# Kernel tuning notes

Measured on AMD Instinct MI355X. Metric: run time of the kernel, lower is better.

Reference implementation:

```python
import jax, jax.numpy as jnp
import numpy as np

THRESHOLD = 0.5
NEG_POS_RATIO = 3
ALPHA = 10.0
N_PRIORS = 8732
N_CLASSES = 21
BATCH = 128
N_OBJ = 32


def cxcy_to_xy(cxcy):
    return jnp.concatenate([cxcy[..., :2] - cxcy[..., 2:] / 2.0,
                            cxcy[..., :2] + cxcy[..., 2:] / 2.0], axis=-1)


def xy_to_cxcy(xy):
    return jnp.concatenate([(xy[..., :2] + xy[..., 2:]) / 2.0,
                            xy[..., 2:] - xy[..., :2]], axis=-1)


def cxcy_to_gcxgcy(cxcy, priors_cxcy):
    return jnp.concatenate([(cxcy[..., :2] - priors_cxcy[..., :2]) / (priors_cxcy[..., 2:] / 10.0),
                            jnp.log(cxcy[..., 2:] / priors_cxcy[..., 2:]) * 5.0], axis=-1)


def find_jaccard_overlap(a, b):
    # a: (M,4) xyxy, b: (P,4) xyxy -> (M,P)
    lt = jnp.maximum(a[:, None, :2], b[None, :, :2])
    rb = jnp.minimum(a[:, None, 2:], b[None, :, 2:])
    wh = jnp.clip(rb - lt, 0.0)
    inter = wh[..., 0] * wh[..., 1]
    area_a = (a[:, 2] - a[:, 0]) * (a[:, 3] - a[:, 1])
    area_b = (b[:, 2] - b[:, 0]) * (b[:, 3] - b[:, 1])
    return inter / (area_a[:, None] + area_b[None, :] - inter)


def _match_one(boxes, labels, priors_xy, priors_cxcy):
    # boxes: (M,4) xyxy, labels: (M,)
    iou = find_jaccard_overlap(boxes, priors_xy)           # (M,P)
    obj_idx = jnp.argmax(iou, axis=1)                      # best prior per object
    iou = iou.at[jnp.arange(boxes.shape[0]), obj_idx].set(1.0)
    positive = (iou >= THRESHOLD).any(axis=0)              # (P,)
    max_prior_idx = jnp.argmax(iou, axis=0)                # best object per prior
    true_cls = labels[max_prior_idx] * positive.astype(labels.dtype)
    matched = boxes[max_prior_idx]                         # (P,4)
    true_locs = cxcy_to_gcxgcy(xy_to_cxcy(matched), priors_cxcy)
    return true_locs, true_cls, positive


def setup_inputs() -> dict:
    key = jax.random.key(0)
    k1, k2, k3, k4, k5, k6 = jax.random.split(key, 6)
    pred_loc = jax.random.normal(k1, (BATCH, N_PRIORS, 4), dtype=jnp.float32)
    pred_cls = jax.random.normal(k2, (BATCH, N_PRIORS, N_CLASSES), dtype=jnp.float32)
    # valid xyxy gt boxes in [0,1]
    p1 = jax.random.uniform(k3, (BATCH, N_OBJ, 2))
    p2 = jax.random.uniform(k4, (BATCH, N_OBJ, 2))
    b_boxes = jnp.concatenate([jnp.minimum(p1, p2), jnp.maximum(p1, p2) + 1e-3], axis=-1)
    b_boxes = jnp.clip(b_boxes, 0.0, 1.0).astype(jnp.float32)
    b_labels = jax.random.randint(k5, (BATCH, N_OBJ), 1, N_CLASSES)
    cxy = jax.random.uniform(k6, (N_PRIORS, 2), minval=0.1, maxval=0.9)
    wh = jax.random.uniform(jax.random.fold_in(k6, 1), (N_PRIORS, 2), minval=0.05, maxval=0.3)
    priors_cxcy = jnp.concatenate([cxy, wh], axis=-1).astype(jnp.float32)
    return {"pred_loc": pred_loc, "pred_cls": pred_cls, "b_boxes": b_boxes,
            "b_labels": b_labels, "priors_cxcy": priors_cxcy}


def reference(pred_loc, pred_cls, b_boxes, b_labels, priors_cxcy):
    batch_size, n_priors, n_classes = pred_cls.shape
    priors_xy = cxcy_to_xy(priors_cxcy)
    true_locs, true_classes, positive = jax.vmap(
        _match_one, in_axes=(0, 0, None, None))(b_boxes, b_labels, priors_xy, priors_cxcy)
    pos_f = positive.astype(pred_loc.dtype)                 # (B,P)
    n_positives = positive.sum(axis=1)                      # (B,)
    n_pos_total = n_positives.sum().astype(pred_loc.dtype)
    # L1 loss (mean over positive box elements)
    loc_loss = (jnp.abs(pred_loc - true_locs) * pos_f[..., None]).sum() / (n_pos_total * 4.0)
    # per-prior cross-entropy
    logp = jax.nn.log_softmax(pred_cls, axis=-1)
    ce = -jnp.take_along_axis(logp, true_classes[..., None], axis=-1)[..., 0]  # (B,P)
    conf_loss_pos = (ce * pos_f).sum()
    # hard negative mining: sort negatives descending per image
    conf_neg = jnp.where(positive, 0.0, ce)
    conf_neg_sorted = -jnp.sort(-conf_neg, axis=1)
    ranks = jnp.arange(n_priors)[None, :]
    hard_mask = ranks < (NEG_POS_RATIO * n_positives)[:, None]
    conf_loss_hard_neg = jnp.where(hard_mask, conf_neg_sorted, 0.0).sum()
    conf_loss = (conf_loss_hard_neg + conf_loss_pos) / n_pos_total
    loc_loss = ALPHA * loc_loss
    total_loss = conf_loss + loc_loss
    return total_loss, loc_loss, conf_loss
```

## Files before the change

### kernel.cpp

```cpp
#include <hip/hip_runtime.h>
#include <math.h>

#define B 128
#define M 32
#define P 8732
#define C 21
#define ALPHA 10.0f
#define NB2 35
#define NSUB 140
#define CH 8
#define CS 1092

typedef float fx4 __attribute__((ext_vector_type(4)));
typedef fx4 fx4u __attribute__((aligned(4)));

#define CE1(val, idx) { float xv_ = (val); se += __expf(xv_); if (cls == (idx)) vc = xv_; }

__global__ __launch_bounds__(256) void k1_partial(
    const float* __restrict__ b_boxes, const float* __restrict__ priors,
    float* __restrict__ pI, float* __restrict__ pU, int* __restrict__ pidx,
    int* __restrict__ done) {
  if (blockIdx.x == 0 && threadIdx.x == 0) *done = 0;
  int b = blockIdx.x >> 3;
  int ch = blockIdx.x & 7;
  int wid = threadIdx.x >> 6;
  int lane = threadIdx.x & 63;
  int obase = wid * 8;

  float ox1[8], oy1[8], ox2[8], oy2[8], oarea[8], bI[8], bU[8];
  int bidx[8];
#pragma unroll
  for (int k = 0; k < 8; k++) {
    float4 bx = ((const float4*)b_boxes)[(size_t)b * M + obase + k];
    ox1[k] = bx.x; oy1[k] = bx.y; ox2[k] = bx.z; oy2[k] = bx.w;
    oarea[k] = (bx.z - bx.x) * (bx.w - bx.y);
    bI[k] = -1.0f; bU[k] = 1.0f; bidx[k] = P;
  }

  int pend = (ch + 1) * CS;
  if (pend > P) pend = P;
#pragma unroll 2
  for (int p = ch * CS + lane; p < pend; p += 64) {
    float4 pr = ((const float4*)priors)[p];
    float pw2 = pr.z * 0.5f, ph2 = pr.w * 0.5f;
    float px1 = pr.x - pw2, py1 = pr.y - ph2;
    float px2 = pr.x + pw2, py2 = pr.y + ph2;
    float areaP = pr.z * pr.w;
#pragma unroll
    for (int k = 0; k < 8; k++) {
      float iw = fminf(ox2[k], px2) - fmaxf(ox1[k], px1);
      float ih = fminf(oy2[k], py2) - fmaxf(oy1[k], py1);
      iw = fmaxf(iw, 0.0f);
      ih = fmaxf(ih, 0.0f);
      float inter = iw * ih;
      float uni = oarea[k] + areaP - inter;
      if (inter * bU[k] > bI[k] * uni) { bI[k] = inter; bU[k] = uni; bidx[k] = p; }
    }
  }
  for (int off = 32; off >= 1; off >>= 1) {
#pragma unroll
    for (int k = 0; k < 8; k++) {
      float oI = __shfl_xor(bI[k], off, 64);
      float oU = __shfl_xor(bU[k], off, 64);
      int oi = __shfl_xor(bidx[k], off, 64);
      float l = oI * bU[k], r = bI[k] * oU;
      if (l > r || (l == r && oi < bidx[k])) { bI[k] = oI; bU[k] = oU; bidx[k] = oi; }
    }
  }
  if (lane == 0) {
#pragma unroll
    for (int k = 0; k < 8; k++) {
      int idx = ((size_t)b * M + obase + k) * CH + ch;
      pI[idx] = bI[k]; pU[idx] = bU[k]; pidx[idx] = bidx[k];
    }
  }
}

template <int KN>
__device__ __forceinline__ void phaseA_group(
    int b, int wid, int lane, int koff, int ntw,
    const float* __restrict__ pred_loc, const float* __restrict__ pred_cls,
    const float* __restrict__ priors,
    const float4* sbox, const int* slab, const int* sobj,
    float* s, float* psl, float* psc, int* psn) {
  float x1[KN], y1[KN], x2[KN], y2[KN], ap[KN];
  float bIr[KN], bUr[KN];
  int bmr[KN], fmr[KN];
#pragma unroll
  for (int j = 0; j < KN; j++) {
    int k = koff + j;
    int p = ((wid + (k << 4)) << 6) + lane;
    x1[j] = 0.0f; y1[j] = 0.0f; x2[j] = 0.0f; y2[j] = 0.0f; ap[j] = 0.0f;
    bIr[j] = -1.0f; bUr[j] = 1.0f; bmr[j] = 0; fmr[j] = 0x7fffffff;
    if (k < ntw && p < P) {
      float4 pr = ((const float4*)priors)[p];
      float pw2 = pr.z * 0.5f, ph2 = pr.w * 0.5f;
      x1[j] = pr.x - pw2; y1[j] = pr.y - ph2;
      x2[j] = pr.x + pw2; y2[j] = pr.y + ph2;
      ap[j] = pr.z * pr.w;
    }
  }
  for (int m = 0; m < M; m++) {
    float4 bx = sbox[m];
    float areaB = (bx.z - bx.x) * (bx.w - bx.y);
    int objm = sobj[m];
#pragma unroll
    for (int j = 0; j < KN; j++) {
      float iw = fminf(bx.z, x2[j]) - fmaxf(bx.x, x1[j]);
      float ih = fminf(bx.w, y2[j]) - fmaxf(bx.y, y1[j]);
      iw = fmaxf(iw, 0.0f);
      ih = fmaxf(ih, 0.0f);
      float inter = iw * ih;
      float uni = areaB + ap[j] - inter;
      if (inter * bUr[j] > bIr[j] * uni) { bIr[j] = inter; bUr[j] = uni; bmr[j] = m; }
      int p = ((wid + ((koff + j) << 4)) << 6) + lane;
      if (fmr[j] == 0x7fffffff && objm == p) fmr[j] = m;
    }
  }
#pragma unroll
  for (int j = 0; j < KN; j++) {
    int k = koff + j;
    if (k < ntw) {
      int t = wid + (k << 4);
      int p = (t << 6) + lane;
      float locpart = 0.0f, cepospart = 0.0f;
      int npos = 0;
      if (p < P) {
        float bIv = bIr[j], bUv = bUr[j];
        int bmv = bmr[j], fmv = fmr[j];
        if (fmv != 0x7fffffff) {
          if (!((bIv == bUv) && (bmv < fmv))) { bIv = 1.0f; bUv = 1.0f; bmv = fmv; }
        }
        bool pos = (2.0f * bIv >= bUv);
        int wAny = __any((int)pos);
        if (wAny) {
          float4 pr = ((const float4*)priors)[p];
          float4 plv = ((const float4*)pred_loc)[(size_t)b * P + p];
          float4 bx = sbox[bmv];
          float cx = (bx.x + bx.z) * 0.5f, cy = (bx.y + bx.w) * 0.5f;
          float w = bx.z - bx.x, h = bx.w - bx.y;
          float rz = __builtin_amdgcn_rcpf(pr.z);
          float rw = __builtin_amdgcn_rcpf(pr.w);
          float g0 = (cx - pr.x) * 10.0f * rz;
          float g1 = (cy - pr.y) * 10.0f * rw;
          float g2 = __logf(w * rz) * 5.0f;
          float g3 = __logf(h * rw) * 5.0f;
          if (pos) {
            locpart = fabsf(plv.x - g0) + fabsf(plv.y - g1) +
                      fabsf(plv.z - g2) + fabsf(plv.w - g3);
            npos = 1;
          }
        }
        int cls = pos ? slab[bmv] : 0;
        const float* uu = pred_cls + ((size_t)b * P + p) * C;
        const fx4u* u4 = (const fx4u*)uu;
        fx4 a0 = u4[0], a1 = u4[1], a2 = u4[2], a3 = u4[3], a4 = u4[4];
        float v20 = uu[20];
        float se = 0.0f, vc = 0.0f;
        CE1(a0.x, 0)  CE1(a0.y, 1)  CE1(a0.z, 2)  CE1(a0.w, 3)
        CE1(a1.x, 4)  CE1(a1.y, 5)  CE1(a1.z, 6)  CE1(a1.w, 7)
        CE1(a2.x, 8)  CE1(a2.y, 9)  CE1(a2.z, 10) CE1(a2.w, 11)
        CE1(a3.x, 12) CE1(a3.y, 13) CE1(a3.z, 14) CE1(a3.w, 15)
        CE1(a4.x, 16) CE1(a4.y, 17) CE1(a4.z, 18) CE1(a4.w, 19)
        CE1(v20, 20)
        float ce = __logf(se) - vc;
        s[p] = pos ? 0.0f : ce;
        cepospart = pos ? ce : 0.0f;
      }
      for (int off = 32; off >= 1; off >>= 1) {
        locpart += __shfl_down(locpart, off, 64);
        cepospart += __shfl_down(cepospart, off, 64);
        npos += __shfl_down(npos, off, 64);
      }
      if (lane == 0) { psl[t] = locpart; psc[t] = cepospart; psn[t] = npos; }
    }
  }
}

__global__ __launch_bounds__(1024) void k23_img(
    const float* __restrict__ pred_loc, const float* __restrict__ pred_cls,
    const float* __restrict__ b_boxes, const int* __restrict__ b_labels,
    const float* __restrict__ priors,
    const float* __restrict__ pI, const float* __restrict__ pU,
    const int* __restrict__ pidx,
    float* __restrict__ imgres, int* __restrict__ done,
    float* __restrict__ out) {
  int b = blockIdx.x;
  int tid = threadIdx.x;
  int wid = tid >> 6;
  int lane = tid & 63;

  __shared__ __align__(16) float s[P];
  __shared__ __align__(16) float4 sbox[M];
  __shared__ int slab[M], sobj[M];
  __shared__ float psl[NSUB], psc[NSUB];
  __shared__ int psn[NSUB];
  __shared__ int histw[16 * 256];
  __shared__ __align__(16) int cnt[256];
  __shared__ int sdig, scum, sK, sLast;
  __shared__ float sLoc, sCe, sNp;
  __shared__ float rsum[16], rl[16], rc[16], rh[16], rn[16];
  __shared__ int rcnt[16];

  if (tid < M) {
    int m = tid;
    float4 bx = ((const float4*)b_boxes)[b * M + m];
    sbox[m] = bx;
    slab[m] = b_labels[b * M + m];
    int o = b * M + m;
    float cI = pI[o * CH], cU = pU[o * CH];
    int ci = pidx[o * CH];
#pragma unroll
    for (int ch = 1; ch < CH; ch++) {
      float nI = pI[o * CH + ch], nU = pU[o * CH + ch];
      int ni = pidx[o * CH + ch];
      if (nI * cU > cI * nU) { cI = nI; cU = nU; ci = ni; }
    }
    sobj[m] = ci;
  }
  __syncthreads();

  int ntw = (wid < 12) ? 9 : 8;
  phaseA_group<5>(b, wid, lane, 0, ntw, pred_loc, pred_cls, priors,
                  sbox, slab, sobj, s, psl, psc, psn);
  phaseA_group<4>(b, wid, lane, 5, ntw, pred_loc, pred_cls, priors,
                  sbox, slab, sobj, s, psl, psc, psn);
  __syncthreads();

  if (wid == 0) {
    float lp = 0.0f, cp = 0.0f;
    int np = 0;
    if (lane < NB2) {
      int t4 = lane * 4;
      lp = ((psl[t4] + psl[t4 + 1]) + psl[t4 + 2]) + psl[t4 + 3];
      cp = ((psc[t4] + psc[t4 + 1]) + psc[t4 + 2]) + psc[t4 + 3];
      np = psn[t4] + psn[t4 + 1] + psn[t4 + 2] + psn[t4 + 3];
    }
    for (int off = 32; off >= 1; off >>= 1) {
      lp += __shfl_down(lp, off, 64);
      cp += __shfl_down(cp, off, 64);
      np += __shfl_down(np, off, 64);
    }
    if (lane == 0) {
      int K = np * 3;
      if (K > P) K = P;
      sK = K; sLoc = lp; sCe = cp; sNp = (float)np;
    }
  }
  __syncthreads();

  int K = sK;
  unsigned pfx = 0;
  int Krem = K;
#pragma unroll
  for (int pass = 3; pass >= 0; --pass) {
    int sh = pass * 8;
    for (int i = tid; i < 16 * 256; i += 1024) histw[i] = 0;
    __syncthreads();
    unsigned himask = (pass == 3) ? 0u : (0xFFFFFFFFu << (sh + 8));
    int* myh = &histw[wid * 256];
    for (int i = tid; i < P; i += 1024) {
      unsigned ub = __float_as_uint(s[i]);
      if ((ub & himask) == pfx) atomicAdd(&myh[(ub >> sh) & 255], 1);
    }
    __syncthreads();
    if (tid < 256) {
      int c = 0;
#pragma unroll
      for (int w = 0; w < 16; w++) c += histw[w * 256 + tid];
      cnt[tid] = c;
    }
    __syncthreads();
    if (wid == 0) {
      int4 c4 = ((const int4*)cnt)[lane];
      int s3 = c4.w;
      int s2 = c4.z + s3;
      int s1 = c4.y + s2;
      int s0 = c4.x + s1;
      int suf = s0;
      for (int off = 1; off < 64; off <<= 1) {
        int t = __shfl_down(suf, off, 64);
        if (lane + off < 64) suf += t;
      }
      int above = suf - s0;
      int S0 = above + s0, S1 = above + s1, S2 = above + s2, S3 = above + s3;
      int S4 = above;
      if (S3 >= Krem && S4 < Krem) { sdig = 4 * lane + 3; scum = S4; }
      else if (S2 >= Krem && S3 < Krem) { sdig = 4 * lane + 2; scum = S3; }
      else if (S1 >= Krem && S2 < Krem) { sdig = 4 * lane + 1; scum = S2; }
      else if (S0 >= Krem && S1 < Krem) { sdig = 4 * lane + 0; scum = S1; }
    }
    __syncthreads();
    pfx |= ((unsigned)sdig) << sh;
    Krem -= scum;
  }
  float tau = __uint_as_float(pfx);

  float sum = 0.0f;
  int cgt = 0;
  for (int i = tid; i < P; i += 1024) {
    float v = s[i];
    if (v > tau) { sum += v; cgt++; }
  }
  for (int off = 32; off >= 1; off >>= 1) {
    sum += __shfl_down(sum, off, 64);
    cgt += __shfl_down(cgt, off, 64);
  }
  if (lane == 0) { rsum[wid] = sum; rcnt[wid] = cgt; }
  __syncthreads();
  if (tid == 0) {
    float stot = 0.0f;
    int ctot = 0;
#pragma unroll
    for (int w = 0; w < 16; w++) { stot += rsum[w]; ctot += rcnt[w]; }
    float hard = stot + (float)(K - ctot) * tau;
    imgres[b * 4 + 0] = sLoc;
    imgres[b * 4 + 1] = sCe;
    imgres[b * 4 + 2] = hard;
    imgres[b * 4 + 3] = sNp;
    __threadfence();
    int prev = atomicAdd(done, 1);
    sLast = (prev == B - 1) ? 1 : 0;
  }
  __syncthreads();
  if (sLast) {
    __threadfence();
    float l = 0.0f, c = 0.0f, h = 0.0f, n = 0.0f;
    if (tid < B) {
      l = atomicAdd(&imgres[tid * 4 + 0], 0.0f);
      c = atomicAdd(&imgres[tid * 4 + 1], 0.0f);
      h = atomicAdd(&imgres[tid * 4 + 2], 0.0f);
      n = atomicAdd(&imgres[tid * 4 + 3], 0.0f);
    }
    for (int off = 32; off >= 1; off >>= 1) {
      l += __shfl_down(l, off, 64);
      c += __shfl_down(c, off, 64);
      h += __shfl_down(h, off, 64);
      n += __shfl_down(n, off, 64);
    }
    if (lane == 0) { rl[wid] = l; rc[wid] = c; rh[wid] = h; rn[wid] = n; }
    __syncthreads();
    if (tid == 0) {
      float L = 0, Cc = 0, H = 0, N = 0;
#pragma unroll
      for (int w = 0; w < 16; w++) { L += rl[w]; Cc += rc[w]; H += rh[w]; N += rn[w]; }
      float loc = ALPHA * L / (N * 4.0f);
      float conf = (H + Cc) / N;
      out[0] = conf + loc;
      out[1] = loc;
      out[2] = conf;
    }
  }
}

extern "C" void kernel_launch(void* const* d_in, const int* in_sizes, int n_in,
                              void* d_out, int out_size, void* d_ws, size_t ws_size,
                              hipStream_t stream) {
  (void)in_sizes; (void)n_in; (void)out_size; (void)ws_size;
  const float* pred_loc = (const float*)d_in[0];
  const float* pred_cls = (const float*)d_in[1];
  const float* b_boxes = (const float*)d_in[2];
  const int* b_labels = (const int*)d_in[3];
  const float* priors = (const float*)d_in[4];
  float* out = (float*)d_out;

  int* done = (int*)d_ws;
  float* imgres = (float*)d_ws + 8;
  float* pI = imgres + B * 4;
  float* pU = pI + B * M * CH;
  int* pidx = (int*)(pU + B * M * CH);

  k1_partial<<<B * CH, 256, 0, stream>>>(b_boxes, priors, pI, pU, pidx, done);
  k23_img<<<B, 1024, 0, stream>>>(pred_loc, pred_cls, b_boxes, b_labels,
                                  priors, pI, pU, pidx, imgres, done, out);
}
```

Baseline: 228.3 us.

## Fuse per-object best-prior search into image kernel and prefetch class logits early

Moves the per-object argmax-over-priors search from a separate 1024-block kernel into the per-image kernel. Partial results now go through shared memory instead of a global workspace, and a tiny init kernel resets the done counter. The pred_cls rows are now loaded up front alongside the priors, before the 32-object IoU loop, so their latency overlaps with compute. Phase A groups are split 3/3/3 to hold the prefetched registers. The risks are higher register pressure and only 128 blocks doing the IoU search, with less parallelism than the old separate kernel.

After: 264.3 us. 15.7% more time.

```diff
diff --git a/kernel.cpp b/kernel.cpp
--- a/kernel.cpp
+++ b/kernel.cpp
@@ -16,64 +16,8 @@
 
 #define CE1(val, idx) { float xv_ = (val); se += __expf(xv_); if (cls == (idx)) vc = xv_; }
 
-__global__ __launch_bounds__(256) void k1_partial(
-    const float* __restrict__ b_boxes, const float* __restrict__ priors,
-    float* __restrict__ pI, float* __restrict__ pU, int* __restrict__ pidx,
-    int* __restrict__ done) {
-  if (blockIdx.x == 0 && threadIdx.x == 0) *done = 0;
-  int b = blockIdx.x >> 3;
-  int ch = blockIdx.x & 7;
-  int wid = threadIdx.x >> 6;
-  int lane = threadIdx.x & 63;
-  int obase = wid * 8;
-
-  float ox1[8], oy1[8], ox2[8], oy2[8], oarea[8], bI[8], bU[8];
-  int bidx[8];
-#pragma unroll
-  for (int k = 0; k < 8; k++) {
-    float4 bx = ((const float4*)b_boxes)[(size_t)b * M + obase + k];
-    ox1[k] = bx.x; oy1[k] = bx.y; ox2[k] = bx.z; oy2[k] = bx.w;
-    oarea[k] = (bx.z - bx.x) * (bx.w - bx.y);
-    bI[k] = -1.0f; bU[k] = 1.0f; bidx[k] = P;
-  }
-
-  int pend = (ch + 1) * CS;
-  if (pend > P) pend = P;
-#pragma unroll 2
-  for (int p = ch * CS + lane; p < pend; p += 64) {
-    float4 pr = ((const float4*)priors)[p];
-    float pw2 = pr.z * 0.5f, ph2 = pr.w * 0.5f;
-    float px1 = pr.x - pw2, py1 = pr.y - ph2;
-    float px2 = pr.x + pw2, py2 = pr.y + ph2;
-    float areaP = pr.z * pr.w;
-#pragma unroll
-    for (int k = 0; k < 8; k++) {
-      float iw = fminf(ox2[k], px2) - fmaxf(ox1[k], px1);
-      float ih = fminf(oy2[k], py2) - fmaxf(oy1[k], py1);
-      iw = fmaxf(iw, 0.0f);
-      ih = fmaxf(ih, 0.0f);
-      float inter = iw * ih;
-      float uni = oarea[k] + areaP - inter;
-      if (inter * bU[k] > bI[k] * uni) { bI[k] = inter; bU[k] = uni; bidx[k] = p; }
-    }
-  }
-  for (int off = 32; off >= 1; off >>= 1) {
-#pragma unroll
-    for (int k = 0; k < 8; k++) {
-      float oI = __shfl_xor(bI[k], off, 64);
-      float oU = __shfl_xor(bU[k], off, 64);
-      int oi = __shfl_xor(bidx[k], off, 64);
-      float l = oI * bU[k], r = bI[k] * oU;
-      if (l > r || (l == r && oi < bidx[k])) { bI[k] = oI; bU[k] = oU; bidx[k] = oi; }
-    }
-  }
-  if (lane == 0) {
-#pragma unroll
-    for (int k = 0; k < 8; k++) {
-      int idx = ((size_t)b * M + obase + k) * CH + ch;
-      pI[idx] = bI[k]; pU[idx] = bU[k]; pidx[idx] = bidx[k];
-    }
-  }
+__global__ void k0_init(int* __restrict__ done) {
+  if (threadIdx.x == 0) *done = 0;
 }
 
 template <int KN>
@@ -86,18 +30,26 @@
   float x1[KN], y1[KN], x2[KN], y2[KN], ap[KN];
   float bIr[KN], bUr[KN];
   int bmr[KN], fmr[KN];
+  fx4 ca[KN], cb[KN], cc[KN], cd[KN], ce4[KN];
+  float c20[KN];
 #pragma unroll
   for (int j = 0; j < KN; j++) {
     int k = koff + j;
     int p = ((wid + (k << 4)) << 6) + lane;
     x1[j] = 0.0f; y1[j] = 0.0f; x2[j] = 0.0f; y2[j] = 0.0f; ap[j] = 0.0f;
     bIr[j] = -1.0f; bUr[j] = 1.0f; bmr[j] = 0; fmr[j] = 0x7fffffff;
+    fx4 z = {0.0f, 0.0f, 0.0f, 0.0f};
+    ca[j] = z; cb[j] = z; cc[j] = z; cd[j] = z; ce4[j] = z; c20[j] = 0.0f;
     if (k < ntw && p < P) {
       float4 pr = ((const float4*)priors)[p];
       float pw2 = pr.z * 0.5f, ph2 = pr.w * 0.5f;
       x1[j] = pr.x - pw2; y1[j] = pr.y - ph2;
       x2[j] = pr.x + pw2; y2[j] = pr.y + ph2;
       ap[j] = pr.z * pr.w;
+      const float* uu = pred_cls + ((size_t)b * P + p) * C;
+      const fx4u* u4 = (const fx4u*)uu;
+      ca[j] = u4[0]; cb[j] = u4[1]; cc[j] = u4[2]; cd[j] = u4[3]; ce4[j] = u4[4];
+      c20[j] = uu[20];
     }
   }
   for (int m = 0; m < M; m++) {
@@ -152,17 +104,13 @@
           }
         }
         int cls = pos ? slab[bmv] : 0;
-        const float* uu = pred_cls + ((size_t)b * P + p) * C;
-        const fx4u* u4 = (const fx4u*)uu;
-        fx4 a0 = u4[0], a1 = u4[1], a2 = u4[2], a3 = u4[3], a4 = u4[4];
-        float v20 = uu[20];
         float se = 0.0f, vc = 0.0f;
-        CE1(a0.x, 0)  CE1(a0.y, 1)  CE1(a0.z, 2)  CE1(a0.w, 3)
-        CE1(a1.x, 4)  CE1(a1.y, 5)  CE1(a1.z, 6)  CE1(a1.w, 7)
-        CE1(a2.x, 8)  CE1(a2.y, 9)  CE1(a2.z, 10) CE1(a2.w, 11)
-        CE1(a3.x, 12) CE1(a3.y, 13) CE1(a3.z, 14) CE1(a3.w, 15)
-        CE1(a4.x, 16) CE1(a4.y, 17) CE1(a4.z, 18) CE1(a4.w, 19)
-        CE1(v20, 20)
+        CE1(ca[j].x, 0)  CE1(ca[j].y, 1)  CE1(ca[j].z, 2)  CE1(ca[j].w, 3)
+        CE1(cb[j].x, 4)  CE1(cb[j].y, 5)  CE1(cb[j].z, 6)  CE1(cb[j].w, 7)
+        CE1(cc[j].x, 8)  CE1(cc[j].y, 9)  CE1(cc[j].z, 10) CE1(cc[j].w, 11)
+        CE1(cd[j].x, 12) CE1(cd[j].y, 13) CE1(cd[j].z, 14) CE1(cd[j].w, 15)
+        CE1(ce4[j].x, 16) CE1(ce4[j].y, 17) CE1(ce4[j].z, 18) CE1(ce4[j].w, 19)
+        CE1(c20[j], 20)
         float ce = __logf(se) - vc;
         s[p] = pos ? 0.0f : ce;
         cepospart = pos ? ce : 0.0f;
@@ -181,8 +129,6 @@
     const float* __restrict__ pred_loc, const float* __restrict__ pred_cls,
     const float* __restrict__ b_boxes, const int* __restrict__ b_labels,
     const float* __restrict__ priors,
-    const float* __restrict__ pI, const float* __restrict__ pU,
-    const int* __restrict__ pidx,
     float* __restrict__ imgres, int* __restrict__ done,
     float* __restrict__ out) {
   int b = blockIdx.x;
@@ -193,6 +139,8 @@
   __shared__ __align__(16) float s[P];
   __shared__ __align__(16) float4 sbox[M];
   __shared__ int slab[M], sobj[M];
+  __shared__ float kIs[M][CH], kUs[M][CH];
+  __shared__ int kix[M][CH];
   __shared__ float psl[NSUB], psc[NSUB];
   __shared__ int psn[NSUB];
   __shared__ int histw[16 * 256];
@@ -207,13 +155,69 @@
     float4 bx = ((const float4*)b_boxes)[b * M + m];
     sbox[m] = bx;
     slab[m] = b_labels[b * M + m];
-    int o = b * M + m;
-    float cI = pI[o * CH], cU = pU[o * CH];
-    int ci = pidx[o * CH];
+  }
+  __syncthreads();
+
+  for (int q = wid; q < 32; q += 16) {
+    int g = q >> 3;
+    int ch = q & 7;
+    int obase = g * 8;
+    float ox1[8], oy1[8], ox2[8], oy2[8], oarea[8], bI[8], bU[8];
+    int bidx[8];
+#pragma unroll
+    for (int k = 0; k < 8; k++) {
+      float4 bx = sbox[obase + k];
+      ox1[k] = bx.x; oy1[k] = bx.y; ox2[k] = bx.z; oy2[k] = bx.w;
+      oarea[k] = (bx.z - bx.x) * (bx.w - bx.y);
+      bI[k] = -1.0f; bU[k] = 1.0f; bidx[k] = P;
+    }
+    int pend = (ch + 1) * CS;
+    if (pend > P) pend = P;
+#pragma unroll 2
+    for (int p = ch * CS + lane; p < pend; p += 64) {
+      float4 pr = ((const float4*)priors)[p];
+      float pw2 = pr.z * 0.5f, ph2 = pr.w * 0.5f;
+      float px1 = pr.x - pw2, py1 = pr.y - ph2;
+      float px2 = pr.x + pw2, py2 = pr.y + ph2;
+      float areaP = pr.z * pr.w;
+#pragma unroll
+      for (int k = 0; k < 8; k++) {
+        float iw = fminf(ox2[k], px2) - fmaxf(ox1[k], px1);
+        float ih = fminf(oy2[k], py2) - fmaxf(oy1[k], py1);
+        iw = fmaxf(iw, 0.0f);
+        ih = fmaxf(ih, 0.0f);
+        float inter = iw * ih;
+        float uni = oarea[k] + areaP - inter;
+        if (inter * bU[k] > bI[k] * uni) { bI[k] = inter; bU[k] = uni; bidx[k] = p; }
+      }
+    }
+    for (int off = 32; off >= 1; off >>= 1) {
+#pragma unroll
+      for (int k = 0; k < 8; k++) {
+        float oI = __shfl_xor(bI[k], off, 64);
+        float oU = __shfl_xor(bU[k], off, 64);
+        int oi = __shfl_xor(bidx[k], off, 64);
+        float l = oI * bU[k], r = bI[k] * oU;
+        if (l > r || (l == r && oi < bidx[k])) { bI[k] = oI; bU[k] = oU; bidx[k] = oi; }
+      }
+    }
+    if (lane == 0) {
+#pragma unroll
+      for (int k = 0; k < 8; k++) {
+        kIs[obase + k][ch] = bI[k]; kUs[obase + k][ch] = bU[k];
+        kix[obase + k][ch] = bidx[k];
+      }
+    }
+  }
+  __syncthreads();
+  if (tid < M) {
+    int m = tid;
+    float cI = kIs[m][0], cU = kUs[m][0];
+    int ci = kix[m][0];
 #pragma unroll
     for (int ch = 1; ch < CH; ch++) {
-      float nI = pI[o * CH + ch], nU = pU[o * CH + ch];
-      int ni = pidx[o * CH + ch];
+      float nI = kIs[m][ch], nU = kUs[m][ch];
+      int ni = kix[m][ch];
       if (nI * cU > cI * nU) { cI = nI; cU = nU; ci = ni; }
     }
     sobj[m] = ci;
@@ -221,9 +225,11 @@
   __syncthreads();
 
   int ntw = (wid < 12) ? 9 : 8;
-  phaseA_group<5>(b, wid, lane, 0, ntw, pred_loc, pred_cls, priors,
+  phaseA_group<3>(b, wid, lane, 0, ntw, pred_loc, pred_cls, priors,
                   sbox, slab, sobj, s, psl, psc, psn);
-  phaseA_group<4>(b, wid, lane, 5, ntw, pred_loc, pred_cls, priors,
+  phaseA_group<3>(b, wid, lane, 3, ntw, pred_loc, pred_cls, priors,
+                  sbox, slab, sobj, s, psl, psc, psn);
+  phaseA_group<3>(b, wid, lane, 6, ntw, pred_loc, pred_cls, priors,
                   sbox, slab, sobj, s, psl, psc, psn);
   __syncthreads();
 
@@ -366,11 +372,8 @@
 
   int* done = (int*)d_ws;
   float* imgres = (float*)d_ws + 8;
-  float* pI = imgres + B * 4;
-  float* pU = pI + B * M * CH;
-  int* pidx = (int*)(pU + B * M * CH);
-
-  k1_partial<<<B * CH, 256, 0, stream>>>(b_boxes, priors, pI, pU, pidx, done);
+
+  k0_init<<<1, 64, 0, stream>>>(done);
   k23_img<<<B, 1024, 0, stream>>>(pred_loc, pred_cls, b_boxes, b_labels,
-                                  priors, pI, pU, pidx, imgres, done, out);
+                                  priors, imgres, done, out);
 }
```
